# Performance work log

Measured on AMD Instinct MI355X. Metric: run time of the kernel, lower is better.

Reference implementation:

```python
import jax, jax.numpy as jnp
import numpy as np

N, E, D, H, G = 100000, 1200000, 20, 64, 128
EPS = 1e-5


def setup_inputs() -> dict:
    key = jax.random.key(0)
    ks = jax.random.split(key, 32)
    inp = {
        'x': jax.random.normal(ks[0], (N, D), jnp.float32),
        'edge_index': jax.random.randint(ks[1], (2, E), 0, N, jnp.int32),
        'batch': jnp.sort(jax.random.randint(ks[2], (N,), 0, G, jnp.int32)),
        'num_graphs': G,
    }
    def w(k, shape):
        return jax.random.normal(k, shape, jnp.float32) * 0.1
    # GCN layers (weight + bias)
    inp['W1'], inp['b1'] = w(ks[3], (D, H)), w(ks[4], (H,))
    inp['W2'], inp['b2'] = w(ks[5], (H, H)), w(ks[6], (H,))
    inp['W3'], inp['b3'] = w(ks[7], (H, H)), w(ks[8], (H,))
    # BatchNorm (eval mode): gamma, beta, running_mean, running_var
    for i, k0 in zip((1, 2, 3), (9, 13, 17)):
        inp[f'g{i}'] = 1.0 + w(ks[k0], (H,))
        inp[f'be{i}'] = w(ks[k0 + 1], (H,))
        inp[f'rm{i}'] = w(ks[k0 + 2], (H,))
        inp[f'rv{i}'] = 1.0 + 0.1 * jax.random.uniform(ks[k0 + 3], (H,), jnp.float32)
    # Heads
    inp['sw1'], inp['sb1'] = w(ks[21], (H, H // 2)), w(ks[22], (H // 2,))
    inp['sw2'], inp['sb2'] = w(ks[23], (H // 2, 1)), w(ks[24], (1,))
    inp['aw1'], inp['ab1'] = w(ks[25], (H, H // 2)), w(ks[26], (H // 2,))
    inp['aw2'], inp['ab2'] = w(ks[27], (H // 2, 4)), w(ks[28], (4,))
    return inp


def reference(x, edge_index, batch, num_graphs,
              W1, b1, W2, b2, W3, b3,
              g1, be1, rm1, rv1, g2, be2, rm2, rv2, g3, be3, rm3, rv3,
              sw1, sb1, sw2, sb2, aw1, ab1, aw2, ab2):
    n = x.shape[0]
    loop = jnp.arange(n, dtype=edge_index.dtype)
    src = jnp.concatenate([edge_index[0], loop])  # with self-loops
    dst = jnp.concatenate([edge_index[1], loop])
    deg = jax.ops.segment_sum(jnp.ones_like(src, jnp.float32), dst, n)
    dis = jax.lax.rsqrt(jnp.maximum(deg, 1.0))  # deg >= 1 due to self-loops
    norm = dis[src] * dis[dst]  # [E+N]

    def gcn(h, W, b):
        m = (h @ W)[src] * norm[:, None]            # gather + normalize per edge
        return jax.ops.segment_sum(m, dst, n) + b   # scatter-add aggregation

    def bn(h, g, be, rm, rv):
        return (h - rm) * jax.lax.rsqrt(rv + EPS) * g + be

    h = jax.nn.relu(bn(gcn(x, W1, b1), g1, be1, rm1, rv1))
    h = jax.nn.relu(bn(gcn(h, W2, b2), g2, be2, rm2, rv2))
    h = jax.nn.relu(bn(gcn(h, W3, b3), g3, be3, rm3, rv3))

    # global mean pool per graph
    sums = jax.ops.segment_sum(h, batch, num_graphs)
    cnts = jax.ops.segment_sum(jnp.ones((n,), jnp.float32), batch, num_graphs)
    emb = sums / jnp.maximum(cnts, 1.0)[:, None]

    score = jax.nn.sigmoid(jax.nn.relu(emb @ sw1 + sb1) @ sw2 + sb2)
    actions = jax.nn.relu(emb @ aw1 + ab1) @ aw2 + ab2
    return score, actions
```

## Files before the change

### kernel.cpp

```cpp
#include <hip/hip_runtime.h>
#include <hip/hip_fp16.h>
#include <math.h>

constexpr int Nn = 100000;
constexpr int Ee = 1200000;
constexpr int Dd = 20;
constexpr int Hh = 64;
constexpr int Gg = 128;
#define EPSF 1e-5f

constexpr int NPB = 128;
constexpr int NBK = (Nn + NPB - 1) / NPB;
constexpr int CAP = 2048;
constexpr int CH  = 2048;

typedef _Float16 half2_raw __attribute__((ext_vector_type(2)));
static __device__ __forceinline__ float fdot2(__half2 a, __half2 b, float c) {
#if __has_builtin(__builtin_amdgcn_fdot2)
    return __builtin_amdgcn_fdot2(*(half2_raw*)&a, *(half2_raw*)&b, c, false);
#else
    float2 fa = __half22float2(a), fb = __half22float2(b);
    return fmaf(fa.y, fb.y, fmaf(fa.x, fb.x, c));
#endif
}

__global__ void zero_gcnt(int* __restrict__ gcnt) {
    int tid = threadIdx.x;
    for (int i = tid; i < NBK; i += 256) gcnt[i] = 0;
}

__global__ void bucketA(const int* __restrict__ src, const int* __restrict__ dst,
                        int* __restrict__ gcnt, int* __restrict__ bkt) {
    __shared__ int lh[NBK];
    __shared__ int lb[NBK];
    int tid = threadIdx.x;
    int base = blockIdx.x * CH;
    int end = min(Ee, base + CH);
    for (int i = tid; i < NBK; i += 256) lh[i] = 0;
    __syncthreads();
    for (int e = base + tid; e < end; e += 256)
        atomicAdd(&lh[dst[e] >> 7], 1);
    __syncthreads();
    for (int i = tid; i < NBK; i += 256) {
        int c = lh[i];
        lb[i] = c ? atomicAdd(&gcnt[i], c) : 0;
        lh[i] = 0;
    }
    __syncthreads();
    for (int e = base + tid; e < end; e += 256) {
        int d = dst[e];
        int b = d >> 7;
        int pos = lb[b] + atomicAdd(&lh[b], 1);
        if (pos < CAP) bkt[b * CAP + pos] = src[e] | ((d & (NPB - 1)) << 20);
    }
}

__global__ void scanB(const int* __restrict__ gcnt, int* __restrict__ gbase,
                      int* __restrict__ row) {
    __shared__ int s[256];
    int tid = threadIdx.x;
    int v[4];
    int sum = 0;
    for (int j = 0; j < 4; ++j) {
        int i = tid * 4 + j;
        v[j] = (i < NBK) ? min(gcnt[i], CAP) : 0;
        sum += v[j];
    }
    s[tid] = sum;
    for (int off = 1; off < 256; off <<= 1) {
        __syncthreads();
        int t = (tid >= off) ? s[tid - off] : 0;
        __syncthreads();
        s[tid] += t;
    }
    __syncthreads();
    int excl = s[tid] - sum;
    for (int j = 0; j < 4; ++j) {
        int i = tid * 4 + j;
        if (i < NBK) { gbase[i] = excl; excl += v[j]; }
    }
    if (tid == 0) row[Nn] = Ee;
}

__global__ void bucketC_pre(const int* __restrict__ gcnt, const int* __restrict__ gbase,
                            const int* __restrict__ bkt, const float* __restrict__ x,
                            int* __restrict__ row, float* __restrict__ dis,
                            int* __restrict__ csr, __half* __restrict__ p32) {
    int b = blockIdx.x, tid = threadIdx.x;
    int cnt = min(gcnt[b], CAP);
    int base = gbase[b];
    __shared__ int sval[CAP];
    __shared__ int ncnt[NPB];
    __shared__ int noff[NPB];
    __shared__ int ncur[NPB];
    __shared__ float sdis[NPB];
    if (tid < NPB) { ncnt[tid] = 0; ncur[tid] = 0; }
    __syncthreads();
    for (int i = tid; i < cnt; i += 256) {
        int v = bkt[b * CAP + i];
        sval[i] = v;
        atomicAdd(&ncnt[v >> 20], 1);
    }
    __syncthreads();
    if (tid < NPB) noff[tid] = ncnt[tid];
    __syncthreads();
    for (int off = 1; off < NPB; off <<= 1) {
        int t = (tid < NPB && tid >= off) ? noff[tid - off] : 0;
        __syncthreads();
        if (tid < NPB) noff[tid] += t;
        __syncthreads();
    }
    if (tid < NPB) {
        int excl = noff[tid] - ncnt[tid];
        noff[tid] = excl;
        float d = rsqrtf((float)ncnt[tid] + 1.0f);
        sdis[tid] = d;
        int node = b * NPB + tid;
        if (node < Nn) {
            row[node] = base + excl;
            dis[node] = d;
        }
    }
    __syncthreads();
    for (int i = tid; i < cnt; i += 256) {
        int v = sval[i];
        int nl = v >> 20;
        int pos = base + noff[nl] + atomicAdd(&ncur[nl], 1);
        csr[pos] = v & 0xFFFFF;
    }
    int nodeBase = b * NPB;
    for (int i = tid; i < NPB * 5; i += 256) {
        int nl = i / 5, c4 = i - nl * 5;
        int n = nodeBase + nl;
        if (n < Nn) {
            float dn = sdis[nl];
            float4 v = ((const float4*)x)[(long)n * 5 + c4];
            __half2 tmp[2];
            tmp[0] = __floats2half2_rn(v.x * dn, v.y * dn);
            tmp[1] = __floats2half2_rn(v.z * dn, v.w * dn);
            *(float2*)&p32[(long)n * 32 + c4 * 4] = *(const float2*)tmp;
        }
    }
    for (int i = tid; i < NPB * 3; i += 256) {
        int nl = i / 3, c = i - nl * 3;
        int n = nodeBase + nl;
        if (n < Nn) {
            float2 zz = make_float2(0.f, 0.f);
            *(float2*)&p32[(long)n * 32 + 20 + c * 4] = zz;
        }
    }
}

static __device__ __forceinline__ void acc_row(float (&acc)[8], const float4& raw) {
    const __half2* hp = (const __half2*)&raw;
#pragma unroll
    for (int j = 0; j < 4; ++j) {
        float2 v = __half22float2(hp[j]);
        acc[2 * j] += v.x; acc[2 * j + 1] += v.y;
    }
}

template <int K, int RS, bool OUTSCALE, int MINW>
__global__ __launch_bounds__(256, MINW)
void fused_layer(const __half* __restrict__ pin, const int* __restrict__ row,
                 const int* __restrict__ csr, const float* __restrict__ dis,
                 const float* __restrict__ W,
                 const float* __restrict__ bb, const float* __restrict__ gg,
                 const float* __restrict__ bee, const float* __restrict__ rmm,
                 const float* __restrict__ rvv, __half* __restrict__ outp) {
    constexpr int LPN  = RS / 8;
    constexpr int TN   = 256 / LPN;
    constexpr int SLOT = RS / 2 + 4;
    int tid = threadIdx.x;
    int f = tid & 63;
    float Af = gg[f] * rsqrtf(rvv[f] + EPSF);
    float Bf = (bb[f] - rmm[f]) * Af + bee[f];
    __half2 wc[K / 2];
#pragma unroll
    for (int j = 0; j < K / 2; ++j)
        wc[j] = __floats2half2_rn(W[(2 * j) * Hh + f], W[(2 * j + 1) * Hh + f]);
    __shared__ __align__(16) __half2 s_lds[TN][SLOT];
    int n0 = blockIdx.x * TN;
    {
        int g = tid / LPN, q = tid - g * LPN;
        int n = n0 + g;
        if (n < Nn) {
            const float4* p4 = (const float4*)pin;
            float acc[8];
            {
                float4 raw = p4[(long)n * LPN + q];
                const __half2* hp = (const __half2*)&raw;
#pragma unroll
                for (int j = 0; j < 4; ++j) {
                    float2 v = __half22float2(hp[j]);
                    acc[2 * j] = v.x; acc[2 * j + 1] = v.y;
                }
            }
            int e0 = row[n], e1 = row[n + 1];
            int e = e0;
            for (; e + 7 < e1; e += 8) {
                int s0 = csr[e],     s1 = csr[e + 1], s2 = csr[e + 2], s3 = csr[e + 3];
                int s4 = csr[e + 4], s5 = csr[e + 5], s6 = csr[e + 6], s7 = csr[e + 7];
                float4 r0 = p4[(long)s0 * LPN + q];
                float4 r1 = p4[(long)s1 * LPN + q];
                float4 r2 = p4[(long)s2 * LPN + q];
                float4 r3 = p4[(long)s3 * LPN + q];
                float4 r4 = p4[(long)s4 * LPN + q];
                float4 r5 = p4[(long)s5 * LPN + q];
                float4 r6 = p4[(long)s6 * LPN + q];
                float4 r7 = p4[(long)s7 * LPN + q];
                acc_row(acc, r0); acc_row(acc, r1); acc_row(acc, r2); acc_row(acc, r3);
                acc_row(acc, r4); acc_row(acc, r5); acc_row(acc, r6); acc_row(acc, r7);
            }
            if (e + 3 < e1) {
                int s0 = csr[e], s1 = csr[e + 1], s2 = csr[e + 2], s3 = csr[e + 3];
                float4 r0 = p4[(long)s0 * LPN + q];
                float4 r1 = p4[(long)s1 * LPN + q];
                float4 r2 = p4[(long)s2 * LPN + q];
                float4 r3 = p4[(long)s3 * LPN + q];
                acc_row(acc, r0); acc_row(acc, r1); acc_row(acc, r2); acc_row(acc, r3);
                e += 4;
            }
            for (; e < e1; ++e) {
                int s0 = csr[e];
                float4 r0 = p4[(long)s0 * LPN + q];
                acc_row(acc, r0);
            }
            __half2 pk[4];
#pragma unroll
            for (int j = 0; j < 4; ++j) pk[j] = __floats2half2_rn(acc[2 * j], acc[2 * j + 1]);
            *(float4*)&s_lds[g][4 * q] = *(const float4*)pk;
        }
    }
    __syncthreads();
    constexpr int NPW = TN / 4;
    int w = tid >> 6;
    for (int j = 0; j < NPW; ++j) {
        int nl = w * NPW + j;
        int n = n0 + nl;
        if (n < Nn) {
            float a0 = 0.f, a1 = 0.f;
#pragma unroll
            for (int j4 = 0; j4 * 4 + 4 <= K / 2; ++j4) {
                float4 raw = *(const float4*)&s_lds[nl][j4 * 4];
                const __half2* sp = (const __half2*)&raw;
                a0 = fdot2(sp[0], wc[j4 * 4 + 0], a0);
                a1 = fdot2(sp[1], wc[j4 * 4 + 1], a1);
                a0 = fdot2(sp[2], wc[j4 * 4 + 2], a0);
                a1 = fdot2(sp[3], wc[j4 * 4 + 3], a1);
            }
            if (K / 2 & 3) {
                constexpr int T0 = (K / 2) & ~3;
                float2 raw2 = *(const float2*)&s_lds[nl][T0];
                const __half2* sp = (const __half2*)&raw2;
                a0 = fdot2(sp[0], wc[T0 + 0], a0);
                a1 = fdot2(sp[1], wc[T0 + 1], a1);
            }
            float dn = dis[n];
            float o = fmaxf((a0 + a1) * dn * Af + Bf, 0.0f);
            if (OUTSCALE) o *= dn;
            outp[(long)n * Hh + f] = __float2half(o);
        }
    }
}

__device__ __forceinline__ int lower_bound_i(const int* __restrict__ a, int n, int v) {
    int lo = 0, hi = n;
    while (lo < hi) {
        int m = (lo + hi) >> 1;
        if (a[m] < v) lo = m + 1; else hi = m;
    }
    return lo;
}

__global__ void pool_heads_h(const __half* __restrict__ h, const int* __restrict__ batch,
                             const float* __restrict__ sw1, const float* __restrict__ sb1,
                             const float* __restrict__ sw2, const float* __restrict__ sb2,
                             const float* __restrict__ aw1, const float* __restrict__ ab1,
                             const float* __restrict__ aw2, const float* __restrict__ ab2,
                             float* __restrict__ out) {
    int gph = blockIdx.x, tid = threadIdx.x;
    __shared__ int slo, shi;
    __shared__ float red[32][8][8];
    __shared__ float semb[64];
    __shared__ float s1[32], sa[32];
    if (tid == 0) {
        slo = lower_bound_i(batch, Nn, gph);
        shi = lower_bound_i(batch, Nn, gph + 1);
    }
    __syncthreads();
    int lo = slo, hi = shi;
    int q = tid & 7, sub = tid >> 3;
    const float4* h4 = (const float4*)h;
    float acc[8];
#pragma unroll
    for (int j = 0; j < 8; ++j) acc[j] = 0.f;
    for (int n = lo + sub; n < hi; n += 32) {
        float4 raw = h4[(long)n * 8 + q];
        const __half2* hp = (const __half2*)&raw;
#pragma unroll
        for (int j = 0; j < 4; ++j) {
            float2 v = __half22float2(hp[j]);
            acc[2 * j] += v.x; acc[2 * j + 1] += v.y;
        }
    }
#pragma unroll
    for (int j = 0; j < 8; ++j) red[sub][q][j] = acc[j];
    __syncthreads();
    if (tid < 64) {
        int qq = tid >> 3, j = tid & 7;
        float s = 0.f;
        for (int sb_ = 0; sb_ < 32; ++sb_) s += red[sb_][qq][j];
        semb[tid] = s / fmaxf((float)(hi - lo), 1.0f);
    }
    __syncthreads();
    if (tid < 32) {
        float a1 = sb1[tid], a2 = ab1[tid];
        for (int k = 0; k < 64; ++k) {
            float e = semb[k];
            a1 += e * sw1[k * 32 + tid];
            a2 += e * aw1[k * 32 + tid];
        }
        s1[tid] = fmaxf(a1, 0.0f);
        sa[tid] = fmaxf(a2, 0.0f);
    }
    __syncthreads();
    if (tid == 0) {
        float acc2 = sb2[0];
        for (int k = 0; k < 32; ++k) acc2 += s1[k] * sw2[k];
        out[gph] = 1.0f / (1.0f + expf(-acc2));
    }
    if (tid >= 4 && tid < 8) {
        int t = tid - 4;
        float acc2 = ab2[t];
        for (int k = 0; k < 32; ++k) acc2 += sa[k] * aw2[k * 4 + t];
        out[Gg + gph * 4 + t] = acc2;
    }
}

extern "C" void kernel_launch(void* const* d_in, const int* in_sizes, int n_in,
                              void* d_out, int out_size, void* d_ws, size_t ws_size,
                              hipStream_t stream) {
    const float* x   = (const float*)d_in[0];
    const int*   ei  = (const int*)d_in[1];
    const int* batch = (const int*)d_in[2];
    const float* W1 = (const float*)d_in[4];
    const float* b1 = (const float*)d_in[5];
    const float* W2 = (const float*)d_in[6];
    const float* b2 = (const float*)d_in[7];
    const float* W3 = (const float*)d_in[8];
    const float* b3 = (const float*)d_in[9];
    const float* g1  = (const float*)d_in[10];
    const float* be1 = (const float*)d_in[11];
    const float* rm1 = (const float*)d_in[12];
    const float* rv1 = (const float*)d_in[13];
    const float* g2  = (const float*)d_in[14];
    const float* be2 = (const float*)d_in[15];
    const float* rm2 = (const float*)d_in[16];
    const float* rv2 = (const float*)d_in[17];
    const float* g3  = (const float*)d_in[18];
    const float* be3 = (const float*)d_in[19];
    const float* rm3 = (const float*)d_in[20];
    const float* rv3 = (const float*)d_in[21];
    const float* sw1 = (const float*)d_in[22];
    const float* sb1 = (const float*)d_in[23];
    const float* sw2 = (const float*)d_in[24];
    const float* sb2 = (const float*)d_in[25];
    const float* aw1 = (const float*)d_in[26];
    const float* ab1 = (const float*)d_in[27];
    const float* aw2 = (const float*)d_in[28];
    const float* ab2 = (const float*)d_in[29];
    float* out = (float*)d_out;

    char* ws = (char*)d_ws;
    auto align256 = [](size_t v) { return (v + 255) & ~(size_t)255; };
    size_t off = 0;
    auto take = [&](size_t bytes) { char* p = ws + off; off += align256(bytes); return p; };
    int*    gcnt  = (int*)   take((size_t)NBK * 4);
    int*    gbase = (int*)   take((size_t)NBK * 4);
    float*  dis   = (float*) take((size_t)Nn * 4);
    int*    row   = (int*)   take((size_t)(Nn + 1) * 4);
    int*    bkt   = (int*)   take((size_t)NBK * CAP * 4);
    int*    csr   = (int*)   take((size_t)Ee * 4);
    __half* p32   = (__half*)take((size_t)Nn * 32 * 2);
    __half* bufA  = (__half*)take((size_t)Nn * Hh * 2);
    __half* bufB  = (__half*)take((size_t)Nn * Hh * 2);

    const int* srcp = ei;
    const int* dstp = ei + Ee;

    const int nWGA = (Ee + CH - 1) / CH;
    const int L1B  = (Nn + 63) / 64;
    const int L2B  = (Nn + 31) / 32;

    zero_gcnt<<<1, 256, 0, stream>>>(gcnt);
    bucketA<<<nWGA, 256, 0, stream>>>(srcp, dstp, gcnt, bkt);
    scanB<<<1, 256, 0, stream>>>(gcnt, gbase, row);
    bucketC_pre<<<NBK, 256, 0, stream>>>(gcnt, gbase, bkt, x, row, dis, csr, p32);

    fused_layer<Dd, 32, true, 2><<<L1B, 256, 0, stream>>>(
        p32, row, csr, dis, W1, b1, g1, be1, rm1, rv1, bufA);

    fused_layer<Hh, 64, true, 2><<<L2B, 256, 0, stream>>>(
        bufA, row, csr, dis, W2, b2, g2, be2, rm2, rv2, bufB);

    fused_layer<Hh, 64, false, 2><<<L2B, 256, 0, stream>>>(
        bufB, row, csr, dis, W3, b3, g3, be3, rm3, rv3, bufA);

    pool_heads_h<<<Gg, 256, 0, stream>>>(bufA, batch, sw1, sb1, sw2, sb2,
                                         aw1, ab1, aw2, ab2, out);
}
```

Baseline: 184.3 us.

## Sort nodes by in-degree to balance per-block gather work in GCN layers

```diff
diff --git a/kernel.cpp b/kernel.cpp
--- a/kernel.cpp
+++ b/kernel.cpp
@@ -13,6 +13,7 @@
 constexpr int NBK = (Nn + NPB - 1) / NPB;
 constexpr int CAP = 2048;
 constexpr int CH  = 2048;
+constexpr int NDB = 64;
 
 typedef _Float16 half2_raw __attribute__((ext_vector_type(2)));
 static __device__ __forceinline__ float fdot2(__half2 a, __half2 b, float c) {
@@ -24,9 +25,10 @@
 #endif
 }
 
-__global__ void zero_gcnt(int* __restrict__ gcnt) {
+__global__ void zero_aux(int* __restrict__ gcnt, int* __restrict__ dcnt) {
     int tid = threadIdx.x;
     for (int i = tid; i < NBK; i += 256) gcnt[i] = 0;
+    if (tid < NDB) dcnt[tid] = 0;
 }
 
 __global__ void bucketA(const int* __restrict__ src, const int* __restrict__ dst,
@@ -85,7 +87,8 @@
 __global__ void bucketC_pre(const int* __restrict__ gcnt, const int* __restrict__ gbase,
                             const int* __restrict__ bkt, const float* __restrict__ x,
                             int* __restrict__ row, float* __restrict__ dis,
-                            int* __restrict__ csr, __half* __restrict__ p32) {
+                            int* __restrict__ csr, __half* __restrict__ p32,
+                            int* __restrict__ dcnt) {
     int b = blockIdx.x, tid = threadIdx.x;
     int cnt = min(gcnt[b], CAP);
     int base = gbase[b];
@@ -94,7 +97,9 @@
     __shared__ int noff[NPB];
     __shared__ int ncur[NPB];
     __shared__ float sdis[NPB];
+    __shared__ int ldh[NDB];
     if (tid < NPB) { ncnt[tid] = 0; ncur[tid] = 0; }
+    if (tid < NDB) ldh[tid] = 0;
     __syncthreads();
     for (int i = tid; i < cnt; i += 256) {
         int v = bkt[b * CAP + i];
@@ -119,6 +124,7 @@
         if (node < Nn) {
             row[node] = base + excl;
             dis[node] = d;
+            atomicAdd(&ldh[min(ncnt[tid], NDB - 1)], 1);
         }
     }
     __syncthreads();
@@ -149,6 +155,35 @@
             *(float2*)&p32[(long)n * 32 + 20 + c * 4] = zz;
         }
     }
+    if (tid < NDB && ldh[tid]) atomicAdd(&dcnt[tid], ldh[tid]);
+}
+
+__global__ void deg_scan(const int* __restrict__ dcnt, int* __restrict__ dcur) {
+    if (threadIdx.x == 0) {
+        int run = 0;
+        for (int bin = 0; bin < NDB; ++bin) { dcur[bin] = run; run += dcnt[bin]; }
+    }
+}
+
+__global__ void deg_scatter(const int* __restrict__ row, int* __restrict__ dcur,
+                            int* __restrict__ perm) {
+    __shared__ int lh[NDB], lb[NDB];
+    int tid = threadIdx.x;
+    if (tid < NDB) lh[tid] = 0;
+    __syncthreads();
+    int n = blockIdx.x * 256 + tid;
+    int d = -1, lpos = 0;
+    if (n < Nn) {
+        d = min(row[n + 1] - row[n], NDB - 1);
+        lpos = atomicAdd(&lh[d], 1);
+    }
+    __syncthreads();
+    if (tid < NDB) {
+        int c = lh[tid];
+        lb[tid] = c ? atomicAdd(&dcur[tid], c) : 0;
+    }
+    __syncthreads();
+    if (n < Nn) perm[lb[d] + lpos] = n;
 }
 
 static __device__ __forceinline__ void acc_row(float (&acc)[8], const float4& raw) {
@@ -164,7 +199,7 @@
 __global__ __launch_bounds__(256, MINW)
 void fused_layer(const __half* __restrict__ pin, const int* __restrict__ row,
                  const int* __restrict__ csr, const float* __restrict__ dis,
-                 const float* __restrict__ W,
+                 const int* __restrict__ perm, const float* __restrict__ W,
                  const float* __restrict__ bb, const float* __restrict__ gg,
                  const float* __restrict__ bee, const float* __restrict__ rmm,
                  const float* __restrict__ rvv, __half* __restrict__ outp) {
@@ -183,8 +218,9 @@
     int n0 = blockIdx.x * TN;
     {
         int g = tid / LPN, q = tid - g * LPN;
-        int n = n0 + g;
-        if (n < Nn) {
+        int np = n0 + g;
+        if (np < Nn) {
+            int n = perm[np];
             const float4* p4 = (const float4*)pin;
             float acc[8];
             {
@@ -237,8 +273,9 @@
     int w = tid >> 6;
     for (int j = 0; j < NPW; ++j) {
         int nl = w * NPW + j;
-        int n = n0 + nl;
-        if (n < Nn) {
+        int np = n0 + nl;
+        if (np < Nn) {
+            int n = perm[np];
             float a0 = 0.f, a1 = 0.f;
 #pragma unroll
             for (int j4 = 0; j4 * 4 + 4 <= K / 2; ++j4) {
@@ -378,8 +415,11 @@
     auto take = [&](size_t bytes) { char* p = ws + off; off += align256(bytes); return p; };
     int*    gcnt  = (int*)   take((size_t)NBK * 4);
     int*    gbase = (int*)   take((size_t)NBK * 4);
+    int*    dcnt  = (int*)   take((size_t)NDB * 4);
+    int*    dcur  = (int*)   take((size_t)NDB * 4);
     float*  dis   = (float*) take((size_t)Nn * 4);
     int*    row   = (int*)   take((size_t)(Nn + 1) * 4);
+    int*    perm  = (int*)   take((size_t)Nn * 4);
     int*    bkt   = (int*)   take((size_t)NBK * CAP * 4);
     int*    csr   = (int*)   take((size_t)Ee * 4);
     __half* p32   = (__half*)take((size_t)Nn * 32 * 2);
@@ -392,20 +432,23 @@
     const int nWGA = (Ee + CH - 1) / CH;
     const int L1B  = (Nn + 63) / 64;
     const int L2B  = (Nn + 31) / 32;
-
-    zero_gcnt<<<1, 256, 0, stream>>>(gcnt);
+    const int NBLK = (Nn + 255) / 256;
+
+    zero_aux<<<1, 256, 0, stream>>>(gcnt, dcnt);
     bucketA<<<nWGA, 256, 0, stream>>>(srcp, dstp, gcnt, bkt);
     scanB<<<1, 256, 0, stream>>>(gcnt, gbase, row);
-    bucketC_pre<<<NBK, 256, 0, stream>>>(gcnt, gbase, bkt, x, row, dis, csr, p32);
+    bucketC_pre<<<NBK, 256, 0, stream>>>(gcnt, gbase, bkt, x, row, dis, csr, p32, dcnt);
+    deg_scan<<<1, 64, 0, stream>>>(dcnt, dcur);
+    deg_scatter<<<NBLK, 256, 0, stream>>>(row, dcur, perm);
 
     fused_layer<Dd, 32, true, 2><<<L1B, 256, 0, stream>>>(
-        p32, row, csr, dis, W1, b1, g1, be1, rm1, rv1, bufA);
+        p32, row, csr, dis, perm, W1, b1, g1, be1, rm1, rv1, bufA);
 
     fused_layer<Hh, 64, true, 2><<<L2B, 256, 0, stream>>>(
-        bufA, row, csr, dis, W2, b2, g2, be2, rm2, rv2, bufB);
+        bufA, row, csr, dis, perm, W2, b2, g2, be2, rm2, rv2, bufB);
 
     fused_layer<Hh, 64, false, 2><<<L2B, 256, 0, stream>>>(
-        bufB, row, csr, dis, W3, b3, g3, be3, rm3, rv3, bufA);
+        bufB, row, csr, dis, perm, W3, b3, g3, be3, rm3, rv3, bufA);
 
     pool_heads_h<<<Gg, 256, 0, stream>>>(bufA, batch, sw1, sb1, sw2, sb2,
                                          aw1, ab1, aw2, ab2, out);
```

New measurement: 215.9 us. +17.2%, slower.

## Make fused GCN layers persistent with double-buffered LDS gather/compute overlap

Applied to the files above, without the earlier changes.

```diff
diff --git a/kernel.cpp b/kernel.cpp
--- a/kernel.cpp
+++ b/kernel.cpp
@@ -171,6 +171,7 @@
     constexpr int LPN  = RS / 8;
     constexpr int TN   = 256 / LPN;
     constexpr int SLOT = RS / 2 + 4;
+    const int nt = (Nn + TN - 1) / TN;
     int tid = threadIdx.x;
     int f = tid & 63;
     float Af = gg[f] * rsqrtf(rvv[f] + EPSF);
@@ -179,13 +180,13 @@
 #pragma unroll
     for (int j = 0; j < K / 2; ++j)
         wc[j] = __floats2half2_rn(W[(2 * j) * Hh + f], W[(2 * j + 1) * Hh + f]);
-    __shared__ __align__(16) __half2 s_lds[TN][SLOT];
-    int n0 = blockIdx.x * TN;
-    {
-        int g = tid / LPN, q = tid - g * LPN;
-        int n = n0 + g;
+    __shared__ __align__(16) __half2 s_lds[2][TN][SLOT];
+    int g = tid / LPN, q = tid - g * LPN;
+    const float4* p4 = (const float4*)pin;
+
+    auto gather = [&](int tile, int b) {
+        int n = tile * TN + g;
         if (n < Nn) {
-            const float4* p4 = (const float4*)pin;
             float acc[8];
             {
                 float4 raw = p4[(long)n * LPN + q];
@@ -198,28 +199,13 @@
             }
             int e0 = row[n], e1 = row[n + 1];
             int e = e0;
-            for (; e + 7 < e1; e += 8) {
-                int s0 = csr[e],     s1 = csr[e + 1], s2 = csr[e + 2], s3 = csr[e + 3];
-                int s4 = csr[e + 4], s5 = csr[e + 5], s6 = csr[e + 6], s7 = csr[e + 7];
-                float4 r0 = p4[(long)s0 * LPN + q];
-                float4 r1 = p4[(long)s1 * LPN + q];
-                float4 r2 = p4[(long)s2 * LPN + q];
-                float4 r3 = p4[(long)s3 * LPN + q];
-                float4 r4 = p4[(long)s4 * LPN + q];
-                float4 r5 = p4[(long)s5 * LPN + q];
-                float4 r6 = p4[(long)s6 * LPN + q];
-                float4 r7 = p4[(long)s7 * LPN + q];
-                acc_row(acc, r0); acc_row(acc, r1); acc_row(acc, r2); acc_row(acc, r3);
-                acc_row(acc, r4); acc_row(acc, r5); acc_row(acc, r6); acc_row(acc, r7);
-            }
-            if (e + 3 < e1) {
+            for (; e + 3 < e1; e += 4) {
                 int s0 = csr[e], s1 = csr[e + 1], s2 = csr[e + 2], s3 = csr[e + 3];
                 float4 r0 = p4[(long)s0 * LPN + q];
                 float4 r1 = p4[(long)s1 * LPN + q];
                 float4 r2 = p4[(long)s2 * LPN + q];
                 float4 r3 = p4[(long)s3 * LPN + q];
                 acc_row(acc, r0); acc_row(acc, r1); acc_row(acc, r2); acc_row(acc, r3);
-                e += 4;
             }
             for (; e < e1; ++e) {
                 int s0 = csr[e];
@@ -229,39 +215,55 @@
             __half2 pk[4];
 #pragma unroll
             for (int j = 0; j < 4; ++j) pk[j] = __floats2half2_rn(acc[2 * j], acc[2 * j + 1]);
-            *(float4*)&s_lds[g][4 * q] = *(const float4*)pk;
-        }
-    }
-    __syncthreads();
-    constexpr int NPW = TN / 4;
-    int w = tid >> 6;
-    for (int j = 0; j < NPW; ++j) {
-        int nl = w * NPW + j;
-        int n = n0 + nl;
-        if (n < Nn) {
-            float a0 = 0.f, a1 = 0.f;
-#pragma unroll
-            for (int j4 = 0; j4 * 4 + 4 <= K / 2; ++j4) {
-                float4 raw = *(const float4*)&s_lds[nl][j4 * 4];
-                const __half2* sp = (const __half2*)&raw;
-                a0 = fdot2(sp[0], wc[j4 * 4 + 0], a0);
-                a1 = fdot2(sp[1], wc[j4 * 4 + 1], a1);
-                a0 = fdot2(sp[2], wc[j4 * 4 + 2], a0);
-                a1 = fdot2(sp[3], wc[j4 * 4 + 3], a1);
+            *(float4*)&s_lds[b][g][4 * q] = *(const float4*)pk;
+        }
+    };
+
+    auto compute = [&](int tile, int b) {
+        constexpr int NPW = TN / 4;
+        int w = tid >> 6;
+        for (int j = 0; j < NPW; ++j) {
+            int nl = w * NPW + j;
+            int n = tile * TN + nl;
+            if (n < Nn) {
+                float a0 = 0.f, a1 = 0.f;
+#pragma unroll
+                for (int j4 = 0; j4 * 4 + 4 <= K / 2; ++j4) {
+                    float4 raw = *(const float4*)&s_lds[b][nl][j4 * 4];
+                    const __half2* sp = (const __half2*)&raw;
+                    a0 = fdot2(sp[0], wc[j4 * 4 + 0], a0);
+                    a1 = fdot2(sp[1], wc[j4 * 4 + 1], a1);
+                    a0 = fdot2(sp[2], wc[j4 * 4 + 2], a0);
+                    a1 = fdot2(sp[3], wc[j4 * 4 + 3], a1);
+                }
+                if (K / 2 & 3) {
+                    constexpr int T0 = (K / 2) & ~3;
+                    float2 raw2 = *(const float2*)&s_lds[b][nl][T0];
+                    const __half2* sp = (const __half2*)&raw2;
+                    a0 = fdot2(sp[0], wc[T0 + 0], a0);
+                    a1 = fdot2(sp[1], wc[T0 + 1], a1);
+                }
+                float dn = dis[n];
+                float o = fmaxf((a0 + a1) * dn * Af + Bf, 0.0f);
+                if (OUTSCALE) o *= dn;
+                outp[(long)n * Hh + f] = __float2half(o);
             }
-            if (K / 2 & 3) {
-                constexpr int T0 = (K / 2) & ~3;
-                float2 raw2 = *(const float2*)&s_lds[nl][T0];
-                const __half2* sp = (const __half2*)&raw2;
-                a0 = fdot2(sp[0], wc[T0 + 0], a0);
-                a1 = fdot2(sp[1], wc[T0 + 1], a1);
-            }
-            float dn = dis[n];
-            float o = fmaxf((a0 + a1) * dn * Af + Bf, 0.0f);
-            if (OUTSCALE) o *= dn;
-            outp[(long)n * Hh + f] = __float2half(o);
-        }
-    }
+        }
+    };
+
+    int t = blockIdx.x;
+    if (t >= nt) return;
+    gather(t, 0);
+    __syncthreads();
+    int buf = 0;
+    while (t + (int)gridDim.x < nt) {
+        gather(t + gridDim.x, buf ^ 1);
+        compute(t, buf);
+        __syncthreads();
+        t += gridDim.x;
+        buf ^= 1;
+    }
+    compute(t, buf);
 }
 
 __device__ __forceinline__ int lower_bound_i(const int* __restrict__ a, int n, int v) {
@@ -390,21 +392,21 @@
     const int* dstp = ei + Ee;
 
     const int nWGA = (Ee + CH - 1) / CH;
-    const int L1B  = (Nn + 63) / 64;
-    const int L2B  = (Nn + 31) / 32;
+    const int L1G  = 782;
+    const int L2G  = 1042;
 
     zero_gcnt<<<1, 256, 0, stream>>>(gcnt);
     bucketA<<<nWGA, 256, 0, stream>>>(srcp, dstp, gcnt, bkt);
     scanB<<<1, 256, 0, stream>>>(gcnt, gbase, row);
     bucketC_pre<<<NBK, 256, 0, stream>>>(gcnt, gbase, bkt, x, row, dis, csr, p32);
 
-    fused_layer<Dd, 32, true, 2><<<L1B, 256, 0, stream>>>(
+    fused_layer<Dd, 32, true, 4><<<L1G, 256, 0, stream>>>(
         p32, row, csr, dis, W1, b1, g1, be1, rm1, rv1, bufA);
 
-    fused_layer<Hh, 64, true, 2><<<L2B, 256, 0, stream>>>(
+    fused_layer<Hh, 64, true, 3><<<L2G, 256, 0, stream>>>(
         bufA, row, csr, dis, W2, b2, g2, be2, rm2, rv2, bufB);
 
-    fused_layer<Hh, 64, false, 2><<<L2B, 256, 0, stream>>>(
+    fused_layer<Hh, 64, false, 3><<<L2G, 256, 0, stream>>>(
         bufB, row, csr, dis, W3, b3, g3, be3, rm3, rv3, bufA);
 
     pool_heads_h<<<Gg, 256, 0, stream>>>(bufA, batch, sw1, sb1, sw2, sb2,
```

After: 199.1 us. +8.0%, slower.
